# Performance work log

Measured on AMD Instinct MI355X. Metric: run time of the kernel, lower is better.

## Reference

```python
import jax, jax.numpy as jnp
import numpy as np

N, E, G = 50000, 800000, 64
DIN, HID, OUT, ED = 128, 64, 96, 32
BN_EPS = 1e-5


def setup_inputs() -> dict:
    key = jax.random.key(0)
    ks = jax.random.split(key, 40)
    d = {}
    d["x"] = jax.random.normal(ks[0], (N, DIN), dtype=jnp.float32)
    d["edge_attr"] = jax.random.normal(ks[1], (E, ED), dtype=jnp.float32)
    d["edge_index"] = jax.random.randint(ks[2], (2, E), 0, N)
    d["batch"] = jnp.sort(jax.random.randint(ks[3], (N,), 0, G))
    dims = [(DIN, HID), (HID, HID), (HID, OUT)]  # (layer input dim, layer output dim)
    i = 4
    for l, (din, dout) in enumerate(dims):
        d[f"le{l}_w"] = jax.random.normal(ks[i], (ED, din), dtype=jnp.float32) * 0.05; i += 1
        d[f"le{l}_b"] = jnp.zeros((din,), dtype=jnp.float32)
        d[f"m{l}_w1"] = jax.random.normal(ks[i], (din, dout), dtype=jnp.float32) * 0.05; i += 1
        d[f"m{l}_b1"] = jnp.zeros((dout,), dtype=jnp.float32)
        d[f"m{l}_w2"] = jax.random.normal(ks[i], (dout, dout), dtype=jnp.float32) * 0.05; i += 1
        d[f"m{l}_b2"] = jnp.zeros((dout,), dtype=jnp.float32)
        d[f"bn{l}_g"] = jnp.ones((dout,), dtype=jnp.float32)
        d[f"bn{l}_b"] = jnp.zeros((dout,), dtype=jnp.float32)
        d[f"bn{l}_m"] = jax.random.normal(ks[i], (dout,), dtype=jnp.float32) * 0.01; i += 1
        d[f"bn{l}_v"] = jnp.ones((dout,), dtype=jnp.float32) + jax.random.uniform(ks[i], (dout,), dtype=jnp.float32) * 0.1; i += 1
    return d


def _gine_layer(x, src, dst, edge_attr, lew, leb, w1, b1, w2, b2,
                bng, bnb, bnm, bnv):
    # GINEConv: message = relu(x_j + Lin(edge_attr)); aggregate = sum into dst
    e = edge_attr @ lew + leb                      # [E, din]
    m = jax.nn.relu(x[src] + e)                    # [E, din]
    agg = jax.ops.segment_sum(m, dst, num_segments=x.shape[0])
    h = x + agg                                    # (1 + eps) * x + agg, eps = 0
    h = jax.nn.relu(h @ w1 + b1) @ w2 + b2         # 2-layer MLP
    # BatchNorm1d (eval: running stats) then ReLU; dropout is identity in eval
    h = (h - bnm) * (bng * jax.lax.rsqrt(bnv + BN_EPS)) + bnb
    return jax.nn.relu(h)


def reference(x, edge_attr,
              le0_w, le0_b, m0_w1, m0_b1, m0_w2, m0_b2, bn0_g, bn0_b, bn0_m, bn0_v,
              le1_w, le1_b, m1_w1, m1_b1, m1_w2, m1_b2, bn1_g, bn1_b, bn1_m, bn1_v,
              le2_w, le2_b, m2_w1, m2_b1, m2_w2, m2_b2, bn2_g, bn2_b, bn2_m, bn2_v,
              edge_index, batch):
    src, dst = edge_index[0], edge_index[1]
    h = _gine_layer(x, src, dst, edge_attr, le0_w, le0_b, m0_w1, m0_b1, m0_w2, m0_b2,
                    bn0_g, bn0_b, bn0_m, bn0_v)
    h = _gine_layer(h, src, dst, edge_attr, le1_w, le1_b, m1_w1, m1_b1, m1_w2, m1_b2,
                    bn1_g, bn1_b, bn1_m, bn1_v)
    h = _gine_layer(h, src, dst, edge_attr, le2_w, le2_b, m2_w1, m2_b1, m2_w2, m2_b2,
                    bn2_g, bn2_b, bn2_m, bn2_v)
    # global mean pool over graphs
    sums = jax.ops.segment_sum(h, batch, num_segments=G)            # [G, OUT]
    cnts = jax.ops.segment_sum(jnp.ones((h.shape[0],), h.dtype), batch, num_segments=G)
    return sums / jnp.maximum(cnts, 1.0)[:, None]
```

## Files before the change

### kernel.cpp

```cpp
#include <hip/hip_runtime.h>
#include <hip/hip_bf16.h>

#define N_NODES 50000
#define N_EDGES 800000
#define N_GRAPHS 64

template <int DIN>
__global__ __launch_bounds__(256) void edge_kernel(
    const float* __restrict__ x, const float* __restrict__ ea,
    const int* __restrict__ ei, const float* __restrict__ lew,
    const float* __restrict__ leb, float* __restrict__ agg, int E) {
  constexpr int FPL = DIN / 64;
  const int lane = threadIdx.x & 63;
  const int wave = __builtin_amdgcn_readfirstlane(threadIdx.x >> 6);
  const int wid = blockIdx.x * (256 >> 6) + wave;
  const int nw = gridDim.x * (256 >> 6);

  float w[32][FPL];
  float bb[FPL];
#pragma unroll
  for (int p = 0; p < FPL; ++p) bb[p] = leb[lane + 64 * p];
#pragma unroll
  for (int k = 0; k < 32; ++k)
#pragma unroll
    for (int p = 0; p < FPL; ++p) w[k][p] = lew[k * DIN + lane + 64 * p];

  const int* __restrict__ srcp = ei;
  const int* __restrict__ dstp = ei + E;

  for (int j = wid; j < E; j += nw) {
    float acc[FPL];
#pragma unroll
    for (int p = 0; p < FPL; ++p) acc[p] = bb[p];
    const float* __restrict__ earow = ea + (size_t)j * 32;
#pragma unroll
    for (int k = 0; k < 32; ++k) {
      float eak = earow[k];
#pragma unroll
      for (int p = 0; p < FPL; ++p) acc[p] = fmaf(eak, w[k][p], acc[p]);
    }
    const int s = srcp[j];
    const int d = dstp[j];
#pragma unroll
    for (int p = 0; p < FPL; ++p) {
      float m = x[(size_t)s * DIN + lane + 64 * p] + acc[p];
      m = m > 0.f ? m : 0.f;
      unsafeAtomicAdd(&agg[(size_t)d * DIN + lane + 64 * p], m);
    }
  }
}

template <int K, int M, bool FUSE_ADD, bool DO_BN>
__global__ void mlp_gemm(const float* __restrict__ in,
                         const float* __restrict__ add,
                         const float* __restrict__ w,
                         const float* __restrict__ bias,
                         const float* __restrict__ bng,
                         const float* __restrict__ bnb,
                         const float* __restrict__ bnm,
                         const float* __restrict__ bnv,
                         float* __restrict__ out, int N) {
  constexpr int Q = M / 4;
  constexpr int NPB = 8;
  __shared__ alignas(16) float ws_[K * M];
  __shared__ alignas(16) float hin[NPB * K];
  __shared__ alignas(16) float bnA[DO_BN ? M : 4];
  __shared__ alignas(16) float bnB[DO_BN ? M : 4];

  const int tid = threadIdx.x;
  const int bdim = Q * NPB;

  for (int i = tid; i < K * M / 4; i += bdim)
    ((float4*)ws_)[i] = ((const float4*)w)[i];
  if constexpr (DO_BN) {
    for (int f = tid; f < M; f += bdim) {
      float s = bng[f] * rsqrtf(bnv[f] + 1e-5f);
      bnA[f] = s;
      bnB[f] = bnb[f] - bnm[f] * s;
    }
  }
  const int nb = blockIdx.x * NPB;
  for (int i = tid; i < NPB * K; i += bdim) {
    const int dn = i / K;
    const int col = i - dn * K;
    const int n = nb + dn;
    float v = 0.f;
    if (n < N) {
      v = in[(size_t)n * K + col];
      if constexpr (FUSE_ADD) v += add[(size_t)n * K + col];
    }
    hin[i] = v;
  }
  __syncthreads();

  const int ns = tid / Q;
  const int q = tid - ns * Q;
  const int n = nb + ns;

  float4 acc = ((const float4*)bias)[q];
#pragma unroll 8
  for (int k = 0; k < K; ++k) {
    const float hv = hin[ns * K + k];
    const float4 wv = ((const float4*)ws_)[k * Q + q];
    acc.x = fmaf(hv, wv.x, acc.x);
    acc.y = fmaf(hv, wv.y, acc.y);
    acc.z = fmaf(hv, wv.z, acc.z);
    acc.w = fmaf(hv, wv.w, acc.w);
  }
  if constexpr (DO_BN) {
    const float4 a = ((const float4*)bnA)[q];
    const float4 b = ((const float4*)bnB)[q];
    acc.x = fmaf(acc.x, a.x, b.x);
    acc.y = fmaf(acc.y, a.y, b.y);
    acc.z = fmaf(acc.z, a.z, b.z);
    acc.w = fmaf(acc.w, a.w, b.w);
  }
  acc.x = acc.x > 0.f ? acc.x : 0.f;
  acc.y = acc.y > 0.f ? acc.y : 0.f;
  acc.z = acc.z > 0.f ? acc.z : 0.f;
  acc.w = acc.w > 0.f ? acc.w : 0.f;
  if (n < N) ((float4*)out)[(size_t)n * Q + q] = acc;
}

__global__ __launch_bounds__(128) void pool_kernel(
    const float* __restrict__ h, const int* __restrict__ batch,
    float* __restrict__ sums, int* __restrict__ cnt, int N) {
  const int f = threadIdx.x;
  const int chunk = (N + gridDim.x - 1) / gridDim.x;
  const int n0 = blockIdx.x * chunk;
  const int n1 = min(n0 + chunk, N);
  int curg = -1;
  float acc = 0.f;
  int c = 0;
  for (int n = n0; n < n1; ++n) {
    const int g = batch[n];
    if (g != curg) {
      if (curg >= 0) {
        if (f < 96) unsafeAtomicAdd(&sums[curg * 96 + f], acc);
        if (f == 0) atomicAdd(&cnt[curg], c);
      }
      curg = g;
      acc = 0.f;
      c = 0;
    }
    if (f < 96) acc += h[(size_t)n * 96 + f];
    ++c;
  }
  if (curg >= 0) {
    if (f < 96) unsafeAtomicAdd(&sums[curg * 96 + f], acc);
    if (f == 0) atomicAdd(&cnt[curg], c);
  }
}

__global__ void finalize_kernel(const float* __restrict__ sums,
                                const int* __restrict__ cnt,
                                float* __restrict__ out) {
  const int i = blockIdx.x * blockDim.x + threadIdx.x;
  if (i < N_GRAPHS * 96) {
    const int g = i / 96;
    const float c = (float)cnt[g];
    out[i] = sums[i] / fmaxf(c, 1.f);
  }
}

extern "C" void kernel_launch(void* const* d_in, const int* in_sizes, int n_in,
                              void* d_out, int out_size, void* d_ws,
                              size_t ws_size, hipStream_t stream) {
  const int N = N_NODES;
  const int E = N_EDGES;

  const float* x = (const float*)d_in[0];
  const float* ea = (const float*)d_in[1];
  const int* ei = (const int*)d_in[2];
  const int* batch = (const int*)d_in[3];
  auto L = [&](int l, int idx) { return (const float*)d_in[4 + 10 * l + idx]; };

  float* ws = (float*)d_ws;
  float* agg = ws;
  float* hA = agg + (size_t)N * 128;
  float* hB = hA + (size_t)N * 96;
  float* t1 = hB + (size_t)N * 64;
  float* sums = t1 + (size_t)N * 96;
  int* cnt = (int*)(sums + N_GRAPHS * 96);

  const int gN8 = (N + 7) / 8;

  hipMemsetAsync(agg, 0, (size_t)N * 128 * 4, stream);
  edge_kernel<128><<<2048, 256, 0, stream>>>(x, ea, ei, L(0, 0), L(0, 1), agg, E);
  mlp_gemm<128, 64, true, false><<<gN8, 128, 0, stream>>>(
      x, agg, L(0, 2), L(0, 3), nullptr, nullptr, nullptr, nullptr, t1, N);
  mlp_gemm<64, 64, false, true><<<gN8, 128, 0, stream>>>(
      t1, nullptr, L(0, 4), L(0, 5), L(0, 6), L(0, 7), L(0, 8), L(0, 9), hA, N);

  hipMemsetAsync(agg, 0, (size_t)N * 64 * 4, stream);
  edge_kernel<64><<<2048, 256, 0, stream>>>(hA, ea, ei, L(1, 0), L(1, 1), agg, E);
  mlp_gemm<64, 64, true, false><<<gN8, 128, 0, stream>>>(
      hA, agg, L(1, 2), L(1, 3), nullptr, nullptr, nullptr, nullptr, t1, N);
  mlp_gemm<64, 64, false, true><<<gN8, 128, 0, stream>>>(
      t1, nullptr, L(1, 4), L(1, 5), L(1, 6), L(1, 7), L(1, 8), L(1, 9), hB, N);

  hipMemsetAsync(agg, 0, (size_t)N * 64 * 4, stream);
  edge_kernel<64><<<2048, 256, 0, stream>>>(hB, ea, ei, L(2, 0), L(2, 1), agg, E);
  mlp_gemm<64, 96, true, false><<<gN8, 192, 0, stream>>>(
      hB, agg, L(2, 2), L(2, 3), nullptr, nullptr, nullptr, nullptr, t1, N);
  mlp_gemm<96, 96, false, true><<<gN8, 192, 0, stream>>>(
      t1, nullptr, L(2, 4), L(2, 5), L(2, 6), L(2, 7), L(2, 8), L(2, 9), hA, N);

  hipMemsetAsync(sums, 0, (size_t)(N_GRAPHS * 96 + N_GRAPHS) * 4, stream);
  pool_kernel<<<512, 128, 0, stream>>>(hA, batch, sums, cnt, N);
  finalize_kernel<<<48, 128, 0, stream>>>(sums, cnt, (float*)d_out);
}
```

Measured before the change: 1.163 ms.

## Replace atomic edge scatter with CSR-by-destination gather aggregation

Builds a destination-sorted CSR (histogram, single-block scan, atomic scatter of edge id/source pairs) once per call. Each layer then uses one wavefront per node, which accumulates relu messages in registers and writes x+agg directly, removing float atomics, the agg memset and the fused add in the first GEMM. The cost is three extra preprocessing kernels, including a serial 1024-thread scan, and load imbalance across nodes with different degrees. Edge attributes are now read in CSR order rather than contiguously.

```diff
diff --git a/kernel.cpp b/kernel.cpp
--- a/kernel.cpp
+++ b/kernel.cpp
@@ -5,16 +5,60 @@
 #define N_EDGES 800000
 #define N_GRAPHS 64
 
+__global__ __launch_bounds__(256) void hist_kernel(const int* __restrict__ ei,
+                                                   int* __restrict__ deg, int E) {
+  int e = blockIdx.x * 256 + threadIdx.x;
+  if (e < E) atomicAdd(&deg[ei[E + e]], 1);
+}
+
+__global__ __launch_bounds__(1024) void scan_kernel(const int* __restrict__ deg,
+                                                    int* __restrict__ row_start,
+                                                    int* __restrict__ cursor, int N) {
+  __shared__ int part[1024];
+  const int t = threadIdx.x;
+  const int C = (N + 1023) / 1024;
+  const int b0 = min(t * C, N);
+  const int b1 = min(b0 + C, N);
+  int s = 0;
+  for (int i = b0; i < b1; ++i) s += deg[i];
+  part[t] = s;
+  __syncthreads();
+  for (int off = 1; off < 1024; off <<= 1) {
+    int v = (t >= off) ? part[t - off] : 0;
+    __syncthreads();
+    part[t] += v;
+    __syncthreads();
+  }
+  int ex = (t == 0) ? 0 : part[t - 1];
+  for (int i = b0; i < b1; ++i) {
+    row_start[i] = ex;
+    cursor[i] = ex;
+    ex += deg[i];
+  }
+  if (t == 1023) row_start[N] = part[1023];
+}
+
+__global__ __launch_bounds__(256) void scatter_kernel(const int* __restrict__ ei,
+                                                      int* __restrict__ cursor,
+                                                      int2* __restrict__ epair, int E) {
+  int e = blockIdx.x * 256 + threadIdx.x;
+  if (e < E) {
+    int d = ei[E + e];
+    int p = atomicAdd(&cursor[d], 1);
+    epair[p] = make_int2(e, ei[e]);
+  }
+}
+
 template <int DIN>
-__global__ __launch_bounds__(256) void edge_kernel(
+__global__ __launch_bounds__(256) void gine_gather(
     const float* __restrict__ x, const float* __restrict__ ea,
-    const int* __restrict__ ei, const float* __restrict__ lew,
-    const float* __restrict__ leb, float* __restrict__ agg, int E) {
+    const int* __restrict__ row_start, const int2* __restrict__ epair,
+    const float* __restrict__ lew, const float* __restrict__ leb,
+    float* __restrict__ hpre, int N) {
   constexpr int FPL = DIN / 64;
   const int lane = threadIdx.x & 63;
-  const int wave = __builtin_amdgcn_readfirstlane(threadIdx.x >> 6);
-  const int wid = blockIdx.x * (256 >> 6) + wave;
-  const int nw = gridDim.x * (256 >> 6);
+  const int wv = __builtin_amdgcn_readfirstlane(blockIdx.x * 4 + (threadIdx.x >> 6));
+  const int nw = gridDim.x * 4;
 
   float w[32][FPL];
   float bb[FPL];
@@ -23,43 +67,50 @@
 #pragma unroll
   for (int k = 0; k < 32; ++k)
 #pragma unroll
-    for (int p = 0; p < FPL; ++p) w[k][p] = lew[k * DIN + lane + 64 * p];
-
-  const int* __restrict__ srcp = ei;
-  const int* __restrict__ dstp = ei + E;
-
-  for (int j = wid; j < E; j += nw) {
+    for (int p = 0; p < FPL; ++p) {
+      w[k][p] = lew[k * DIN + lane + 64 * p];
+      asm("" : "+v"(w[k][p]));
+    }
+
+  for (int n = wv; n < N; n += nw) {
+    const int e0 = row_start[n];
+    const int e1 = row_start[n + 1];
     float acc[FPL];
 #pragma unroll
-    for (int p = 0; p < FPL; ++p) acc[p] = bb[p];
-    const float* __restrict__ earow = ea + (size_t)j * 32;
-#pragma unroll
-    for (int k = 0; k < 32; ++k) {
-      float eak = earow[k];
-#pragma unroll
-      for (int p = 0; p < FPL; ++p) acc[p] = fmaf(eak, w[k][p], acc[p]);
-    }
-    const int s = srcp[j];
-    const int d = dstp[j];
-#pragma unroll
-    for (int p = 0; p < FPL; ++p) {
-      float m = x[(size_t)s * DIN + lane + 64 * p] + acc[p];
-      m = m > 0.f ? m : 0.f;
-      unsafeAtomicAdd(&agg[(size_t)d * DIN + lane + 64 * p], m);
-    }
-  }
-}
-
-template <int K, int M, bool FUSE_ADD, bool DO_BN>
-__global__ void mlp_gemm(const float* __restrict__ in,
-                         const float* __restrict__ add,
-                         const float* __restrict__ w,
-                         const float* __restrict__ bias,
-                         const float* __restrict__ bng,
-                         const float* __restrict__ bnb,
-                         const float* __restrict__ bnm,
-                         const float* __restrict__ bnv,
-                         float* __restrict__ out, int N) {
+    for (int p = 0; p < FPL; ++p) acc[p] = 0.f;
+
+    for (int i = e0; i < e1; ++i) {
+      const int2 es = epair[i];
+      const int e = __builtin_amdgcn_readfirstlane(es.x);
+      const int s = __builtin_amdgcn_readfirstlane(es.y);
+      const float* __restrict__ earow = ea + (size_t)e * 32;
+      float t[FPL];
+#pragma unroll
+      for (int p = 0; p < FPL; ++p) t[p] = bb[p];
+#pragma unroll
+      for (int k = 0; k < 32; ++k) {
+        const float eak = earow[k];
+#pragma unroll
+        for (int p = 0; p < FPL; ++p) t[p] = fmaf(eak, w[k][p], t[p]);
+      }
+#pragma unroll
+      for (int p = 0; p < FPL; ++p) {
+        const float m = t[p] + x[(size_t)s * DIN + lane + 64 * p];
+        acc[p] += fmaxf(m, 0.f);
+      }
+    }
+#pragma unroll
+    for (int p = 0; p < FPL; ++p)
+      hpre[(size_t)n * DIN + lane + 64 * p] =
+          x[(size_t)n * DIN + lane + 64 * p] + acc[p];
+  }
+}
+
+template <int K, int M, bool DO_BN>
+__global__ void mlp_gemm(const float* __restrict__ in, const float* __restrict__ w,
+                         const float* __restrict__ bias, const float* __restrict__ bng,
+                         const float* __restrict__ bnb, const float* __restrict__ bnm,
+                         const float* __restrict__ bnv, float* __restrict__ out, int N) {
   constexpr int Q = M / 4;
   constexpr int NPB = 8;
   __shared__ alignas(16) float ws_[K * M];
@@ -84,12 +135,7 @@
     const int dn = i / K;
     const int col = i - dn * K;
     const int n = nb + dn;
-    float v = 0.f;
-    if (n < N) {
-      v = in[(size_t)n * K + col];
-      if constexpr (FUSE_ADD) v += add[(size_t)n * K + col];
-    }
-    hin[i] = v;
+    hin[i] = (n < N) ? in[(size_t)n * K + col] : 0.f;
   }
   __syncthreads();
 
@@ -122,9 +168,10 @@
   if (n < N) ((float4*)out)[(size_t)n * Q + q] = acc;
 }
 
-__global__ __launch_bounds__(128) void pool_kernel(
-    const float* __restrict__ h, const int* __restrict__ batch,
-    float* __restrict__ sums, int* __restrict__ cnt, int N) {
+__global__ __launch_bounds__(128) void pool_kernel(const float* __restrict__ h,
+                                                   const int* __restrict__ batch,
+                                                   float* __restrict__ sums,
+                                                   int* __restrict__ cnt, int N) {
   const int f = threadIdx.x;
   const int chunk = (N + gridDim.x - 1) / gridDim.x;
   const int n0 = blockIdx.x * chunk;
@@ -153,8 +200,7 @@
 }
 
 __global__ void finalize_kernel(const float* __restrict__ sums,
-                                const int* __restrict__ cnt,
-                                float* __restrict__ out) {
+                                const int* __restrict__ cnt, float* __restrict__ out) {
   const int i = blockIdx.x * blockDim.x + threadIdx.x;
   if (i < N_GRAPHS * 96) {
     const int g = i / 96;
@@ -164,8 +210,8 @@
 }
 
 extern "C" void kernel_launch(void* const* d_in, const int* in_sizes, int n_in,
-                              void* d_out, int out_size, void* d_ws,
-                              size_t ws_size, hipStream_t stream) {
+                              void* d_out, int out_size, void* d_ws, size_t ws_size,
+                              hipStream_t stream) {
   const int N = N_NODES;
   const int E = N_EDGES;
 
@@ -175,36 +221,45 @@
   const int* batch = (const int*)d_in[3];
   auto L = [&](int l, int idx) { return (const float*)d_in[4 + 10 * l + idx]; };
 
-  float* ws = (float*)d_ws;
-  float* agg = ws;
-  float* hA = agg + (size_t)N * 128;
+  int* iws = (int*)d_ws;
+  int* deg = iws;
+  int* row_start = deg + N;
+  int* cursor = row_start + N + 1;
+  int2* epair = (int2*)(iws + 150004);
+  float* fws = (float*)(iws + 150004 + 2 * E);
+  float* hpre = fws;
+  float* t1 = hpre + (size_t)N * 128;
+  float* hA = t1 + (size_t)N * 96;
   float* hB = hA + (size_t)N * 96;
-  float* t1 = hB + (size_t)N * 64;
-  float* sums = t1 + (size_t)N * 96;
+  float* sums = hB + (size_t)N * 64;
   int* cnt = (int*)(sums + N_GRAPHS * 96);
 
+  const int gE = (E + 255) / 256;
+  const int gW = (N + 3) / 4;
   const int gN8 = (N + 7) / 8;
 
-  hipMemsetAsync(agg, 0, (size_t)N * 128 * 4, stream);
-  edge_kernel<128><<<2048, 256, 0, stream>>>(x, ea, ei, L(0, 0), L(0, 1), agg, E);
-  mlp_gemm<128, 64, true, false><<<gN8, 128, 0, stream>>>(
-      x, agg, L(0, 2), L(0, 3), nullptr, nullptr, nullptr, nullptr, t1, N);
-  mlp_gemm<64, 64, false, true><<<gN8, 128, 0, stream>>>(
-      t1, nullptr, L(0, 4), L(0, 5), L(0, 6), L(0, 7), L(0, 8), L(0, 9), hA, N);
-
-  hipMemsetAsync(agg, 0, (size_t)N * 64 * 4, stream);
-  edge_kernel<64><<<2048, 256, 0, stream>>>(hA, ea, ei, L(1, 0), L(1, 1), agg, E);
-  mlp_gemm<64, 64, true, false><<<gN8, 128, 0, stream>>>(
-      hA, agg, L(1, 2), L(1, 3), nullptr, nullptr, nullptr, nullptr, t1, N);
-  mlp_gemm<64, 64, false, true><<<gN8, 128, 0, stream>>>(
-      t1, nullptr, L(1, 4), L(1, 5), L(1, 6), L(1, 7), L(1, 8), L(1, 9), hB, N);
-
-  hipMemsetAsync(agg, 0, (size_t)N * 64 * 4, stream);
-  edge_kernel<64><<<2048, 256, 0, stream>>>(hB, ea, ei, L(2, 0), L(2, 1), agg, E);
-  mlp_gemm<64, 96, true, false><<<gN8, 192, 0, stream>>>(
-      hB, agg, L(2, 2), L(2, 3), nullptr, nullptr, nullptr, nullptr, t1, N);
-  mlp_gemm<96, 96, false, true><<<gN8, 192, 0, stream>>>(
-      t1, nullptr, L(2, 4), L(2, 5), L(2, 6), L(2, 7), L(2, 8), L(2, 9), hA, N);
+  hipMemsetAsync(deg, 0, (size_t)N * 4, stream);
+  hist_kernel<<<gE, 256, 0, stream>>>(ei, deg, E);
+  scan_kernel<<<1, 1024, 0, stream>>>(deg, row_start, cursor, N);
+  scatter_kernel<<<gE, 256, 0, stream>>>(ei, cursor, epair, E);
+
+  gine_gather<128><<<gW, 256, 0, stream>>>(x, ea, row_start, epair, L(0, 0), L(0, 1), hpre, N);
+  mlp_gemm<128, 64, false><<<gN8, 128, 0, stream>>>(
+      hpre, L(0, 2), L(0, 3), nullptr, nullptr, nullptr, nullptr, t1, N);
+  mlp_gemm<64, 64, true><<<gN8, 128, 0, stream>>>(
+      t1, L(0, 4), L(0, 5), L(0, 6), L(0, 7), L(0, 8), L(0, 9), hA, N);
+
+  gine_gather<64><<<gW, 256, 0, stream>>>(hA, ea, row_start, epair, L(1, 0), L(1, 1), hpre, N);
+  mlp_gemm<64, 64, false><<<gN8, 128, 0, stream>>>(
+      hpre, L(1, 2), L(1, 3), nullptr, nullptr, nullptr, nullptr, t1, N);
+  mlp_gemm<64, 64, true><<<gN8, 128, 0, stream>>>(
+      t1, L(1, 4), L(1, 5), L(1, 6), L(1, 7), L(1, 8), L(1, 9), hB, N);
+
+  gine_gather<64><<<gW, 256, 0, stream>>>(hB, ea, row_start, epair, L(2, 0), L(2, 1), hpre, N);
+  mlp_gemm<64, 96, false><<<gN8, 192, 0, stream>>>(
+      hpre, L(2, 2), L(2, 3), nullptr, nullptr, nullptr, nullptr, t1, N);
+  mlp_gemm<96, 96, true><<<gN8, 192, 0, stream>>>(
+      t1, L(2, 4), L(2, 5), L(2, 6), L(2, 7), L(2, 8), L(2, 9), hA, N);
 
   hipMemsetAsync(sums, 0, (size_t)(N_GRAPHS * 96 + N_GRAPHS) * 4, stream);
   pool_kernel<<<512, 128, 0, stream>>>(hA, batch, sums, cnt, N);
```

New measurement: 978.3 us. -15.9%, faster.
